# Kernel optimization log

Hardware: AMD Instinct MI355X
Metric: run time of the kernel (lower is better)

The kernel has to match this reference:

```python
import jax, jax.numpy as jnp
import numpy as np

E = 1024      # embed_dim
H = 16        # num_heads
D = E // H    # head_dim
T = 2048      # tgt_len
S = 2048      # src_len
B = 8         # batch
SCALE = D ** -0.5
EPS = 1e-6


def setup_inputs() -> dict:
    key = jax.random.key(0)
    ks = jax.random.split(key, 8)
    w = lambda k: jax.random.normal(k, (E, E), jnp.float32) * (1.0 / np.sqrt(E))
    return {
        "query": jax.random.normal(ks[0], (T, B, E), jnp.float32),
        "key_in": jax.random.normal(ks[1], (S, B, E), jnp.float32),
        "value": jax.random.normal(ks[2], (S, B, E), jnp.float32),
        "wq": w(ks[3]), "bq": jnp.zeros((E,), jnp.float32),
        "wk": w(ks[4]), "bk": jnp.zeros((E,), jnp.float32),
        "wv": w(ks[5]), "bv": jnp.zeros((E,), jnp.float32),
        "wo": w(ks[6]), "bo": jnp.zeros((E,), jnp.float32),
    }


def _to_heads(x):
    # (L, B, E) -> (B*H, L, D), matching fairseq's view/transpose
    L = x.shape[0]
    return x.reshape(L, B * H, D).transpose(1, 0, 2)


def reference(query, key_in, value, wq, bq, wk, bk, wv, bv, wo, bo):
    # projections (fairseq scales q by head_dim**-0.5)
    q = (query @ wq.T + bq) * SCALE
    k = key_in @ wk.T + bk
    v = value @ wv.T + bv
    # cosFormer feature map: ReLU then cos/sin positional reweighting
    q = jax.nn.relu(_to_heads(q))   # (BH, T, D)
    k = jax.nn.relu(_to_heads(k))   # (BH, S, D)
    v = _to_heads(v)                # (BH, S, D)
    # sin(pi/2 * i / len), cos(pi/2 * i / len) for i in 1..len
    iq = jnp.arange(1, T + 1, dtype=jnp.float32) / T
    ik = jnp.arange(1, S + 1, dtype=jnp.float32) / S
    half_pi = jnp.float32(np.pi / 2)
    sq = jnp.sin(half_pi * iq)[None, :, None]
    cq = jnp.cos(half_pi * iq)[None, :, None]
    sk = jnp.sin(half_pi * ik)[None, :, None]
    ck = jnp.cos(half_pi * ik)[None, :, None]
    q2 = jnp.concatenate([q * sq, q * cq], axis=-1)   # (BH, T, 2D)
    k2 = jnp.concatenate([k * sk, k * ck], axis=-1)   # (BH, S, 2D)
    # linear attention: O(S*D^2) instead of O(S^2*D)
    kv = jnp.einsum('bsd,bse->bde', k2, v)            # (BH, 2D, D)
    num = jnp.einsum('btd,bde->bte', q2, kv)          # (BH, T, D)
    den = jnp.einsum('btd,bd->bt', q2, k2.sum(axis=1))
    out = num / jnp.maximum(den, EPS)[..., None]
    out = out.transpose(1, 0, 2).reshape(T, B, E)     # back to (T, B, E)
    return out @ wo.T + bo
```

## Files before the change

kernel.cpp:

```cpp
#include <hip/hip_runtime.h>
#include <hip/hip_bf16.h>

using bf16 = __hip_bfloat16;
typedef __attribute__((ext_vector_type(8))) short short8;
typedef __attribute__((ext_vector_type(4))) float f32x4;

#define GLL16(gp, lp) __builtin_amdgcn_global_load_lds( \
    (__attribute__((address_space(1))) void*)(gp),      \
    (__attribute__((address_space(3))) void*)(lp), 16, 0, 0)

__device__ __forceinline__ bf16 f2b(float x) { return __float2bfloat16(x); }
__device__ __forceinline__ float s2f(short x) {
  unsigned u = ((unsigned)(unsigned short)x) << 16;
  return __uint_as_float(u);
}
__device__ __forceinline__ short f2s(float x) {
  bf16 h = __float2bfloat16(x);
  return *reinterpret_cast<short*>(&h);
}

#define TRIG_C (1.5707963268f / 2048.0f)

__global__ void cvt_f32_bf16(const float* __restrict__ src, bf16* __restrict__ dst, int n8)
{
  const int i = blockIdx.x * 256 + threadIdx.x;
  if (i >= n8) return;
  const f32x4 a = ((const f32x4*)src)[i * 2];
  const f32x4 b = ((const f32x4*)src)[i * 2 + 1];
  short8 o;
#pragma unroll
  for (int j = 0; j < 4; ++j) { o[j] = f2s(a[j]); o[4 + j] = f2s(b[j]); }
  *(short8*)&dst[i * 8] = o;
}

template<int MODE>
__global__ __launch_bounds__(512, 2)
void proj_gemm(const bf16* __restrict__ A, const bf16* __restrict__ W,
               const float* __restrict__ bias, void* __restrict__ O)
{
  constexpr int K = 1024;
  constexpr int BK = 64;
  extern __shared__ __align__(16) char smem[];
  bf16* lds = (bf16*)smem;

  const int tid = threadIdx.x;
  const int w = tid >> 6, l = tid & 63;
  const int quad = l >> 4, l16 = l & 15;
  const int lrow = l >> 3;
  const int scol = ((l & 7) ^ lrow) << 3;
  const int wm = w >> 2, wn = w & 3;

  const int bid = blockIdx.x;
  const int xcd = bid & 7, idx = bid >> 3;
  const int ni = idx & 3;
  const int mi = xcd + 8 * (idx >> 2);
  const long mblk = (long)mi * 256;
  const int  nblk = ni * 256;
  const bf16* Ag = A + mblk * K;
  const bf16* Wg = W + (long)nblk * K;

  f32x4 acc[8][4] = {};

  auto STAGE = [&](int buf, int kt) {
    bf16* As = lds + buf * 32768;
    bf16* Bs = As + 16384;
#pragma unroll
    for (int i = 0; i < 4; ++i) {
      const int c = w * 4 + i;
      const int r = c * 8 + lrow;
      GLL16(Ag + (long)r * K + kt + scol, &As[c * 512]);
      GLL16(Wg + (long)r * K + kt + scol, &Bs[c * 512]);
    }
  };

  STAGE(0, 0);
  __syncthreads();

  for (int t = 0; t < K / BK; ++t) {
    if (t + 1 < K / BK) STAGE((t + 1) & 1, (t + 1) * BK);
    const bf16* As = lds + (t & 1) * 32768;
    const bf16* Bs = As + 16384;
#pragma unroll
    for (int kk = 0; kk < BK; kk += 32) {
      const int ko8 = (kk + quad * 8) >> 3;
      short8 a[8], b[4];
#pragma unroll
      for (int sb = 0; sb < 8; ++sb) {
        const int row = wm * 128 + sb * 16 + l16;
        a[sb] = *(const short8*)&As[row * 64 + ((ko8 ^ (row & 7)) << 3)];
      }
#pragma unroll
      for (int u = 0; u < 4; ++u) {
        const int row = wn * 64 + u * 16 + l16;
        b[u] = *(const short8*)&Bs[row * 64 + ((ko8 ^ (row & 7)) << 3)];
      }
#pragma unroll
      for (int sb = 0; sb < 8; ++sb)
#pragma unroll
        for (int u = 0; u < 4; ++u)
          acc[sb][u] = __builtin_amdgcn_mfma_f32_16x16x32_bf16(a[sb], b[u], acc[sb][u], 0, 0, 0);
    }
    __syncthreads();
  }

  if (MODE == 3) {
#pragma unroll
    for (int sb = 0; sb < 8; ++sb) {
      const int row0 = (int)mblk + wm * 128 + sb * 16 + quad * 4;
#pragma unroll
      for (int u = 0; u < 4; ++u) {
        const int col = nblk + wn * 64 + u * 16 + l16;
        const float bc = bias[col];
#pragma unroll
        for (int j = 0; j < 4; ++j)
          ((float*)O)[(long)(row0 + j) * 1024 + col] = acc[sb][u][j] + bc;
      }
    }
  } else {
    bf16* T = lds;
#pragma unroll
    for (int sb = 0; sb < 8; ++sb) {
#pragma unroll
      for (int u = 0; u < 4; ++u) {
        const int lc = wn * 64 + u * 16 + l16;
        const int h = lc >> 6, d = lc & 63;
        const float bc = bias[nblk + lc];
#pragma unroll
        for (int j = 0; j < 4; ++j) {
          const int lr = wm * 128 + sb * 16 + quad * 4 + j;
          float v = acc[sb][u][j] + bc;
          if (MODE == 0) v = fmaxf(v * 0.125f, 0.f);
          if (MODE == 1) v = fmaxf(v, 0.f);
          int ix;
          if (MODE == 0) {
            const int tt = lr >> 3, bb = lr & 7;
            const int dc = (d >> 3) ^ (tt & 7);
            ix = (((bb * 4 + h) * 32 + tt) * 8 + dc) * 8 + (d & 7);
          } else {
            const int ss = lr >> 3, bb = lr & 7;
            const int sc = (ss >> 3) ^ (d & 3);
            ix = (((bb * 4 + h) * 64 + d) * 4 + sc) * 8 + (ss & 7);
          }
          T[ix] = f2b(v);
        }
      }
    }
    __syncthreads();
    const int hbase = nblk >> 6;
    const int sbase = (int)(mblk >> 3);
#pragma unroll
    for (int i = 0; i < 16; ++i) {
      const int c = i * 512 + tid;
      if (MODE == 0) {
        const int dch = c & 7, tt = (c >> 3) & 31, h = (c >> 8) & 3, bb = c >> 10;
        const short8 val = *(const short8*)&T[(((bb * 4 + h) * 32 + tt) * 8 + (dch ^ (tt & 7))) * 8];
        bf16* dst = (bf16*)O + ((long)(bb * 16 + hbase + h) * 2048 + sbase + tt) * 64 + dch * 8;
        *(short8*)dst = val;
      } else {
        const int sc = c & 3, d = (c >> 2) & 63, h = (c >> 8) & 3, bb = c >> 10;
        const short8 val = *(const short8*)&T[(((bb * 4 + h) * 64 + d) * 4 + (sc ^ (d & 3))) * 8];
        bf16* dst = (bf16*)O + ((long)(bb * 16 + hbase + h) * 64 + d) * 2048 + sbase + sc * 8;
        *(short8*)dst = val;
      }
    }
  }
}

__global__ void kv_gemm(const bf16* __restrict__ VhT, const bf16* __restrict__ KhT,
                        bf16* __restrict__ kv2, float* __restrict__ ksum2)
{
  __shared__ __align__(16) bf16 Vs[2][64 * 64];
  __shared__ __align__(16) bf16 Ks[2][64 * 64];
  const int bh = blockIdx.x;
  const int fl = blockIdx.y;
  const int tid = threadIdx.x, w = tid >> 6, l = tid & 63;
  const int quad = l >> 4, l16 = l & 15;
  const int lrow = l >> 3;
  const int scol = ((l & 7) ^ lrow) << 3;
  const bf16* Vg = VhT + (long)bh * 64 * 2048;
  const bf16* Kg = KhT + (long)bh * 64 * 2048;
  const int ar = tid >> 2, ac8 = (tid & 3) * 2;
  const int r7 = ar & 7;

  f32x4 acc[4] = {};
  float ps = 0.f;

  auto VSTAGE = [&](int buf, int kt) {
#pragma unroll
    for (int i = 0; i < 2; ++i) {
      const int c = w * 2 + i, r = c * 8 + lrow;
      GLL16(Vg + (long)r * 2048 + kt + scol, &Vs[buf][c * 512]);
    }
  };
  auto KLOAD = [&](int kt, short8& ka, short8& kb) {
    ka = *(const short8*)&Kg[(long)ar * 2048 + kt + ac8 * 8];
    kb = *(const short8*)&Kg[(long)ar * 2048 + kt + ac8 * 8 + 8];
  };
  auto KSCALE = [&](int buf, int kt, short8 ka, short8 kb) {
    short8 o0, o1;
#pragma unroll
    for (int j = 0; j < 8; ++j) {
      const int sA = kt + ac8 * 8 + j, sB = sA + 8;
      const float angA = (float)(sA + 1) * TRIG_C, angB = (float)(sB + 1) * TRIG_C;
      const float wA = fl ? __cosf(angA) : __sinf(angA);
      const float wB = fl ? __cosf(angB) : __sinf(angB);
      const float fA = s2f(ka[j]), fB = s2f(kb[j]);
      o0[j] = f2s(fA * wA);  o1[j] = f2s(fB * wB);
      ps += fA * wA + fB * wB;
    }
    *(short8*)&Ks[buf][ar * 64 + ((ac8 ^ r7) << 3)]       = o0;
    *(short8*)&Ks[buf][ar * 64 + (((ac8 + 1) ^ r7) << 3)] = o1;
  };

  { short8 ka, kb; KLOAD(0, ka, kb); VSTAGE(0, 0); KSCALE(0, 0, ka, kb); }
  __syncthreads();

  for (int t = 0; t < 32; ++t) {
    short8 ka, kb;
    if (t < 31) { KLOAD((t + 1) * 64, ka, kb); VSTAGE((t + 1) & 1, (t + 1) * 64); }
    const int buf = t & 1;
#pragma unroll
    for (int kk = 0; kk < 64; kk += 32) {
      const int ko8 = (kk + quad * 8) >> 3;
      const int rowa = w * 16 + l16;
      short8 a = *(const short8*)&Vs[buf][rowa * 64 + ((ko8 ^ (l16 & 7)) << 3)];
      short8 b[4];
#pragma unroll
      for (int u = 0; u < 4; ++u)
        b[u] = *(const short8*)&Ks[buf][(u * 16 + l16) * 64 + ((ko8 ^ (l16 & 7)) << 3)];
#pragma unroll
      for (int tn = 0; tn < 4; ++tn)
        acc[tn] = __builtin_amdgcn_mfma_f32_16x16x32_bf16(a, b[tn], acc[tn], 0, 0, 0);
    }
    if (t < 31) KSCALE((t + 1) & 1, (t + 1) * 64, ka, kb);
    __syncthreads();
  }

  bf16* out = kv2 + (long)bh * 128 * 64 + fl * 64 * 64;
#pragma unroll
  for (int tn = 0; tn < 4; ++tn) {
    const int d = tn * 16 + l16;
#pragma unroll
    for (int j = 0; j < 4; ++j) {
      const int e = w * 16 + quad * 4 + j;
      out[e * 64 + d] = f2b(acc[tn][j]);
    }
  }
  ps += __shfl_xor(ps, 1);
  ps += __shfl_xor(ps, 2);
  if ((tid & 3) == 0) ksum2[bh * 128 + fl * 64 + ar] = ps;
}

__global__ void attn_out(const bf16* __restrict__ Qh, const bf16* __restrict__ kv2,
                         const float* __restrict__ ksum2g, bf16* __restrict__ att)
{
  __shared__ __align__(16) bf16 Qs[128 * 64];
  __shared__ __align__(16) bf16 Ks[128 * 64];
  __shared__ float ks[128];
  __shared__ float dinv_s[128];
  const int bh = blockIdx.y;
  const int t0 = blockIdx.x * 128;
  const int tid = threadIdx.x, w = tid >> 6, l = tid & 63;
  const int quad = l >> 4, l16 = l & 15;
  const int lrow = l >> 3;
  const int scol = ((l & 7) ^ lrow) << 3;
  const bf16* Qg = Qh + ((long)bh * 2048 + t0) * 64;
  const bf16* Kg = kv2 + (long)bh * 128 * 64;
#pragma unroll
  for (int i = 0; i < 4; ++i) {
    const int c = w * 4 + i, r = c * 8 + lrow;
    GLL16(Qg + (long)r * 64 + scol, &Qs[c * 512]);
  }
#pragma unroll
  for (int i = 0; i < 4; ++i) {
    const int c = w * 4 + i, r = c * 8 + lrow;
    GLL16(Kg + (long)r * 64 + scol, &Ks[c * 512]);
  }
  if (tid < 128) ks[tid] = ksum2g[bh * 128 + tid];
  __syncthreads();

  {
    const int r = tid >> 1, half = tid & 1;
    float d1 = 0.f, d2 = 0.f;
#pragma unroll
    for (int blk = 0; blk < 4; ++blk) {
      const int g = (half * 4 + blk) ^ (r & 7);
      const short8 v = *(const short8*)&Qs[r * 64 + g * 8];
#pragma unroll
      for (int j = 0; j < 8; ++j) {
        const float f = s2f(v[j]);
        const int d = half * 32 + blk * 8 + j;
        d1 += f * ks[d];
        d2 += f * ks[64 + d];
      }
    }
    d1 += __shfl_xor(d1, 1);
    d2 += __shfl_xor(d2, 1);
    if (half == 0) {
      const float ang = (float)(t0 + r + 1) * TRIG_C;
      const float den = __sinf(ang) * d1 + __cosf(ang) * d2;
      dinv_s[r] = 1.f / fmaxf(den, 1e-6f);
    }
  }

  f32x4 accs[2][4] = {}, accc[2][4] = {};
#pragma unroll
  for (int kk = 0; kk < 64; kk += 32) {
    const int ko8 = (kk + quad * 8) >> 3;
    short8 a[2], bs[4], bc[4];
#pragma unroll
    for (int u = 0; u < 2; ++u) {
      const int row = w * 32 + u * 16 + l16;
      a[u] = *(const short8*)&Qs[row * 64 + ((ko8 ^ (row & 7)) << 3)];
    }
#pragma unroll
    for (int u = 0; u < 4; ++u) {
      bs[u] = *(const short8*)&Ks[(u * 16 + l16) * 64 + ((ko8 ^ (l16 & 7)) << 3)];
      bc[u] = *(const short8*)&Ks[(64 + u * 16 + l16) * 64 + ((ko8 ^ (l16 & 7)) << 3)];
    }
#pragma unroll
    for (int tm = 0; tm < 2; ++tm)
#pragma unroll
      for (int tn = 0; tn < 4; ++tn) {
        accs[tm][tn] = __builtin_amdgcn_mfma_f32_16x16x32_bf16(a[tm], bs[tn], accs[tm][tn], 0, 0, 0);
        accc[tm][tn] = __builtin_amdgcn_mfma_f32_16x16x32_bf16(a[tm], bc[tn], accc[tm][tn], 0, 0, 0);
      }
  }
  __syncthreads();

  const int bb = bh >> 4, h = bh & 15;
#pragma unroll
  for (int tm = 0; tm < 2; ++tm)
#pragma unroll
    for (int j = 0; j < 4; ++j) {
      const int tr = w * 32 + tm * 16 + quad * 4 + j;
      const int t = t0 + tr;
      const float di = dinv_s[tr];
      const float ang = (float)(t + 1) * TRIG_C;
      const float sn = __sinf(ang), cs = __cosf(ang);
#pragma unroll
      for (int tn = 0; tn < 4; ++tn) {
        const int e = tn * 16 + l16;
        const float v = (sn * accs[tm][tn][j] + cs * accc[tm][tn][j]) * di;
        att[((long)t * 8 + bb) * 1024 + h * 64 + e] = f2b(v);
      }
    }
}

extern "C" void kernel_launch(void* const* d_in, const int* in_sizes, int n_in,
                              void* d_out, int out_size, void* d_ws, size_t ws_size,
                              hipStream_t stream)
{
  const float* query  = (const float*)d_in[0];
  const float* key_in = (const float*)d_in[1];
  const float* value  = (const float*)d_in[2];
  const float* wq = (const float*)d_in[3];  const float* bq = (const float*)d_in[4];
  const float* wk = (const float*)d_in[5];  const float* bk = (const float*)d_in[6];
  const float* wv = (const float*)d_in[7];  const float* bv = (const float*)d_in[8];
  const float* wo = (const float*)d_in[9];  const float* bo = (const float*)d_in[10];

  char* ws = (char*)d_ws;
  float* ksum2 = (float*)(ws);
  bf16*  kv2   = (bf16*)(ws + 1114112);
  bf16*  Wslot = (bf16*)(ws + 3211264);
  bf16*  R1    = (bf16*)(ws + 5308416);
  bf16*  KhT = R1, *ATT = R1;
  bf16*  D1 = (bf16*)d_out;
  bf16*  D2 = (bf16*)d_out + 16777216;

  const int PROJ_LDS = 131072;
  hipFuncSetAttribute((const void*)&proj_gemm<0>, hipFuncAttributeMaxDynamicSharedMemorySize, PROJ_LDS);
  hipFuncSetAttribute((const void*)&proj_gemm<1>, hipFuncAttributeMaxDynamicSharedMemorySize, PROJ_LDS);
  hipFuncSetAttribute((const void*)&proj_gemm<2>, hipFuncAttributeMaxDynamicSharedMemorySize, PROJ_LDS);
  hipFuncSetAttribute((const void*)&proj_gemm<3>, hipFuncAttributeMaxDynamicSharedMemorySize, PROJ_LDS);

  dim3 blk(256);
  dim3 pblk(512);
  dim3 gproj(256);
  const int nBig = 16777216 / 8, gBig = nBig / 256;
  const int nW   = 1048576 / 8,  gW   = nW / 256;

  hipLaunchKernelGGL(cvt_f32_bf16, dim3(gBig), blk, 0, stream, key_in, D1, nBig);
  hipLaunchKernelGGL(cvt_f32_bf16, dim3(gW),   blk, 0, stream, wk, Wslot, nW);
  hipLaunchKernelGGL((proj_gemm<1>), gproj, pblk, PROJ_LDS, stream, D1, Wslot, bk, KhT);
  hipLaunchKernelGGL(cvt_f32_bf16, dim3(gBig), blk, 0, stream, value, D2, nBig);
  hipLaunchKernelGGL(cvt_f32_bf16, dim3(gW),   blk, 0, stream, wv, Wslot, nW);
  hipLaunchKernelGGL((proj_gemm<2>), gproj, pblk, PROJ_LDS, stream, D2, Wslot, bv, D1);
  hipLaunchKernelGGL(kv_gemm, dim3(128, 2), blk, 0, stream, D1, KhT, kv2, ksum2);
  hipLaunchKernelGGL(cvt_f32_bf16, dim3(gBig), blk, 0, stream, query, D2, nBig);
  hipLaunchKernelGGL(cvt_f32_bf16, dim3(gW),   blk, 0, stream, wq, Wslot, nW);
  hipLaunchKernelGGL((proj_gemm<0>), gproj, pblk, PROJ_LDS, stream, D2, Wslot, bq, D1);
  hipLaunchKernelGGL(attn_out, dim3(16, 128), blk, 0, stream, D1, kv2, ksum2, ATT);
  hipLaunchKernelGGL(cvt_f32_bf16, dim3(gW),   blk, 0, stream, wo, Wslot, nW);
  hipLaunchKernelGGL((proj_gemm<3>), gproj, pblk, PROJ_LDS, stream, ATT, Wslot, bo, d_out);
}
```

Measured before the change: 439.1 us.

## Fuse fp32-to-bf16 conversion into projection GEMM loads

Removes the standalone f32->bf16 conversion kernels for the activations and weights. The projection GEMM now loads fp32 data into registers, converts it to bf16 and writes it to LDS itself, so the load of the next tile overlaps the MFMA work on the current one. This drops a full write and read of the bf16 intermediates and several kernel launches. In exchange the GEMM reads twice as many bytes from global memory, and the weights are converted again by every block, which adds register pressure and VALU work inside the main loop.

```diff
diff --git a/kernel.cpp b/kernel.cpp
--- a/kernel.cpp
+++ b/kernel.cpp
@@ -21,25 +21,15 @@
 
 #define TRIG_C (1.5707963268f / 2048.0f)
 
-__global__ void cvt_f32_bf16(const float* __restrict__ src, bf16* __restrict__ dst, int n8)
-{
-  const int i = blockIdx.x * 256 + threadIdx.x;
-  if (i >= n8) return;
-  const f32x4 a = ((const f32x4*)src)[i * 2];
-  const f32x4 b = ((const f32x4*)src)[i * 2 + 1];
-  short8 o;
-#pragma unroll
-  for (int j = 0; j < 4; ++j) { o[j] = f2s(a[j]); o[4 + j] = f2s(b[j]); }
-  *(short8*)&dst[i * 8] = o;
-}
-
 template<int MODE>
 __global__ __launch_bounds__(512, 2)
-void proj_gemm(const bf16* __restrict__ A, const bf16* __restrict__ W,
+void proj_gemm(const void* __restrict__ Ain, const float* __restrict__ Wf,
                const float* __restrict__ bias, void* __restrict__ O)
 {
   constexpr int K = 1024;
   constexpr int BK = 64;
+  constexpr int NT = K / BK;
+  constexpr bool AF32 = (MODE != 3);
   extern __shared__ __align__(16) char smem[];
   bf16* lds = (bf16*)smem;
 
@@ -56,29 +46,51 @@
   const int mi = xcd + 8 * (idx >> 2);
   const long mblk = (long)mi * 256;
   const int  nblk = ni * 256;
-  const bf16* Ag = A + mblk * K;
-  const bf16* Wg = W + (long)nblk * K;
+
+  const float* Af = (const float*)Ain + mblk * K;
+  const bf16*  Ab = (const bf16*)Ain  + mblk * K;
+  const float* Wg = Wf + (long)nblk * K;
 
   f32x4 acc[8][4] = {};
-
-  auto STAGE = [&](int buf, int kt) {
+  f32x4 pa0[4], pa1[4];
+  f32x4 pw0[4], pw1[4];
+
+  auto LOADS = [&](int buf, int kt) {
+#pragma unroll
+    for (int i = 0; i < 4; ++i) {
+      const int c = w * 4 + i, r = c * 8 + lrow;
+      if (AF32) {
+        const float* s = Af + (long)r * K + kt + (l & 7) * 8;
+        pa0[i] = *(const f32x4*)s;
+        pa1[i] = *(const f32x4*)(s + 4);
+      } else {
+        GLL16(Ab + (long)r * K + kt + scol, &lds[buf * 32768 + c * 512]);
+      }
+      const float* sw = Wg + (long)r * K + kt + (l & 7) * 8;
+      pw0[i] = *(const f32x4*)sw;
+      pw1[i] = *(const f32x4*)(sw + 4);
+    }
+  };
+  auto WRITES = [&](int buf) {
     bf16* As = lds + buf * 32768;
     bf16* Bs = As + 16384;
 #pragma unroll
     for (int i = 0; i < 4; ++i) {
-      const int c = w * 4 + i;
-      const int r = c * 8 + lrow;
-      GLL16(Ag + (long)r * K + kt + scol, &As[c * 512]);
-      GLL16(Wg + (long)r * K + kt + scol, &Bs[c * 512]);
-    }
-  };
-
-  STAGE(0, 0);
-  __syncthreads();
-
-  for (int t = 0; t < K / BK; ++t) {
-    if (t + 1 < K / BK) STAGE((t + 1) & 1, (t + 1) * BK);
-    const bf16* As = lds + (t & 1) * 32768;
+      const int c = w * 4 + i, r = c * 8 + lrow;
+      if (AF32) {
+        short8 o;
+#pragma unroll
+        for (int j = 0; j < 4; ++j) { o[j] = f2s(pa0[i][j]); o[4 + j] = f2s(pa1[i][j]); }
+        *(short8*)&As[r * 64 + scol] = o;
+      }
+      short8 ow;
+#pragma unroll
+      for (int j = 0; j < 4; ++j) { ow[j] = f2s(pw0[i][j]); ow[4 + j] = f2s(pw1[i][j]); }
+      *(short8*)&Bs[r * 64 + scol] = ow;
+    }
+  };
+  auto COMPUTE = [&](int buf) {
+    const bf16* As = lds + buf * 32768;
     const bf16* Bs = As + 16384;
 #pragma unroll
     for (int kk = 0; kk < BK; kk += 32) {
@@ -100,6 +112,16 @@
         for (int u = 0; u < 4; ++u)
           acc[sb][u] = __builtin_amdgcn_mfma_f32_16x16x32_bf16(a[sb], b[u], acc[sb][u], 0, 0, 0);
     }
+  };
+
+  LOADS(0, 0);
+  WRITES(0);
+  __syncthreads();
+
+  for (int t = 0; t < NT; ++t) {
+    if (t + 1 < NT) LOADS((t + 1) & 1, (t + 1) * BK);
+    COMPUTE(t & 1);
+    if (t + 1 < NT) WRITES((t + 1) & 1);
     __syncthreads();
   }
 
@@ -362,7 +384,6 @@
   char* ws = (char*)d_ws;
   float* ksum2 = (float*)(ws);
   bf16*  kv2   = (bf16*)(ws + 1114112);
-  bf16*  Wslot = (bf16*)(ws + 3211264);
   bf16*  R1    = (bf16*)(ws + 5308416);
   bf16*  KhT = R1, *ATT = R1;
   bf16*  D1 = (bf16*)d_out;
@@ -377,20 +398,11 @@
   dim3 blk(256);
   dim3 pblk(512);
   dim3 gproj(256);
-  const int nBig = 16777216 / 8, gBig = nBig / 256;
-  const int nW   = 1048576 / 8,  gW   = nW / 256;
-
-  hipLaunchKernelGGL(cvt_f32_bf16, dim3(gBig), blk, 0, stream, key_in, D1, nBig);
-  hipLaunchKernelGGL(cvt_f32_bf16, dim3(gW),   blk, 0, stream, wk, Wslot, nW);
-  hipLaunchKernelGGL((proj_gemm<1>), gproj, pblk, PROJ_LDS, stream, D1, Wslot, bk, KhT);
-  hipLaunchKernelGGL(cvt_f32_bf16, dim3(gBig), blk, 0, stream, value, D2, nBig);
-  hipLaunchKernelGGL(cvt_f32_bf16, dim3(gW),   blk, 0, stream, wv, Wslot, nW);
-  hipLaunchKernelGGL((proj_gemm<2>), gproj, pblk, PROJ_LDS, stream, D2, Wslot, bv, D1);
+
+  hipLaunchKernelGGL((proj_gemm<1>), gproj, pblk, PROJ_LDS, stream, key_in, wk, bk, KhT);
+  hipLaunchKernelGGL((proj_gemm<2>), gproj, pblk, PROJ_LDS, stream, value,  wv, bv, D1);
   hipLaunchKernelGGL(kv_gemm, dim3(128, 2), blk, 0, stream, D1, KhT, kv2, ksum2);
-  hipLaunchKernelGGL(cvt_f32_bf16, dim3(gBig), blk, 0, stream, query, D2, nBig);
-  hipLaunchKernelGGL(cvt_f32_bf16, dim3(gW),   blk, 0, stream, wq, Wslot, nW);
-  hipLaunchKernelGGL((proj_gemm<0>), gproj, pblk, PROJ_LDS, stream, D2, Wslot, bq, D1);
-  hipLaunchKernelGGL(attn_out, dim3(16, 128), blk, 0, stream, D1, kv2, ksum2, ATT);
-  hipLaunchKernelGGL(cvt_f32_bf16, dim3(gW),   blk, 0, stream, wo, Wslot, nW);
-  hipLaunchKernelGGL((proj_gemm<3>), gproj, pblk, PROJ_LDS, stream, ATT, Wslot, bo, d_out);
-}
+  hipLaunchKernelGGL((proj_gemm<0>), gproj, pblk, PROJ_LDS, stream, query,  wq, bq, D2);
+  hipLaunchKernelGGL(attn_out, dim3(16, 128), blk, 0, stream, D2, kv2, ksum2, ATT);
+  hipLaunchKernelGGL((proj_gemm<3>), gproj, pblk, PROJ_LDS, stream, ATT, wo, bo, d_out);
+}
```

Result: slower. 488.7 us (+11.3%).
